# Performance work log

Measured on AMD Instinct MI355X. Metric: run time of the kernel, lower is better.

Reference implementation:

```python
import jax, jax.numpy as jnp
import numpy as np

B, E, H, L, V = 128, 1024, 1024, 2, 32001  # vocab = output_size + 1
PAD_IDX = 1000


def gru_cell(x, h, w_ih, w_hh, b_ih, b_hh):
    # PyTorch GRU cell math; gates ordered (r, z, n)
    gi = x @ w_ih.T + b_ih            # [B, 3H]
    gh = h @ w_hh.T + b_hh            # [B, 3H]
    i_r, i_z, i_n = jnp.split(gi, 3, axis=-1)
    h_r, h_z, h_n = jnp.split(gh, 3, axis=-1)
    r = jax.nn.sigmoid(i_r + h_r)
    z = jax.nn.sigmoid(i_z + h_z)
    n = jnp.tanh(i_n + r * h_n)
    return (1.0 - z) * n + z * h


def setup_inputs() -> dict:
    key = jax.random.key(0)
    ks = jax.random.split(key, 16)
    input_vector = jax.random.randint(ks[0], (B,), 0, V)
    hidden = jax.random.normal(ks[1], (L, B, H), dtype=jnp.float32)
    emb = jax.random.uniform(ks[2], (V, E), minval=-0.1, maxval=0.1, dtype=jnp.float32)
    emb = emb.at[PAD_IDX].set(0.0)  # padding_idx
    s = 1.0 / np.sqrt(H)
    def u(k, shape):
        return jax.random.uniform(k, shape, minval=-s, maxval=s, dtype=jnp.float32)
    w_ih0 = u(ks[3], (3 * H, E)); w_hh0 = u(ks[4], (3 * H, H))
    b_ih0 = u(ks[5], (3 * H,));  b_hh0 = u(ks[6], (3 * H,))
    w_ih1 = u(ks[7], (3 * H, H)); w_hh1 = u(ks[8], (3 * H, H))
    b_ih1 = u(ks[9], (3 * H,));  b_hh1 = u(ks[10], (3 * H,))
    w_out = jax.random.uniform(ks[11], (V, H), minval=-0.1, maxval=0.1, dtype=jnp.float32)
    b_out = jnp.zeros((V,), dtype=jnp.float32)
    return dict(input_vector=input_vector, hidden=hidden, emb=emb,
                w_ih0=w_ih0, w_hh0=w_hh0, b_ih0=b_ih0, b_hh0=b_hh0,
                w_ih1=w_ih1, w_hh1=w_hh1, b_ih1=b_ih1, b_hh1=b_hh1,
                w_out=w_out, b_out=b_out)


def reference(input_vector, hidden, emb, w_ih0, w_hh0, b_ih0, b_hh0,
              w_ih1, w_hh1, b_ih1, b_hh1, w_out, b_out):
    x = jax.nn.relu(emb[input_vector])          # [B, E] (seq_len=1 squeezed)
    h0 = gru_cell(x, hidden[0], w_ih0, w_hh0, b_ih0, b_hh0)   # [B, H]
    h1 = gru_cell(h0, hidden[1], w_ih1, w_hh1, b_ih1, b_hh1)  # [B, H]
    logits = h1 @ w_out.T + b_out               # [B, V]
    out = jax.nn.log_softmax(logits, axis=-1)   # [B, V]
    hidden_out = jnp.stack([h0, h1], axis=0)    # [L, B, H]
    return out, hidden_out
```

## Files before the change

### kernel.cpp

```cpp
#include <hip/hip_runtime.h>
#include <cmath>

#define BATCH 128
#define KDIM 1024
#define VOCAB 32001
#define G3 3072
#define GIP_STRIDE (BATCH * G3)

typedef __bf16 bf16_t;
typedef bf16_t bf16x8 __attribute__((ext_vector_type(8)));
typedef float f32x4 __attribute__((ext_vector_type(4)));

__device__ __forceinline__ void stage16(const float* g, void* lds_wave_base) {
    __builtin_amdgcn_global_load_lds(
        (const __attribute__((address_space(1))) void*)g,
        (__attribute__((address_space(3))) void*)lds_wave_base, 16, 0, 0);
}

template<bool RELU>
__device__ __forceinline__ bf16x8 frag_from_lds(const float* s, int row, int quad) {
    const int s7 = row & 7;
    f32x4 u = *(const f32x4*)(s + row * 32 + (((2 * quad) ^ s7) * 4));
    f32x4 v = *(const f32x4*)(s + row * 32 + (((2 * quad + 1) ^ s7) * 4));
    if (RELU) {
#pragma unroll
        for (int k = 0; k < 4; ++k) { u[k] = fmaxf(u[k], 0.f); v[k] = fmaxf(v[k], 0.f); }
    }
    bf16x8 r;
    r[0] = (bf16_t)u[0]; r[1] = (bf16_t)u[1]; r[2] = (bf16_t)u[2]; r[3] = (bf16_t)u[3];
    r[4] = (bf16_t)v[0]; r[5] = (bf16_t)v[1]; r[6] = (bf16_t)v[2]; r[7] = (bf16_t)v[3];
    return r;
}

template<bool GATHER>
__device__ __forceinline__ void gemm128_core(
    const float* __restrict__ Abase, const int* __restrict__ idx,
    const float* __restrict__ W, const float* __restrict__ bias,
    float* __restrict__ C, int ldc, int Wrows, int n0, int kbeg, int kend)
{
    __shared__ float sA[2][128 * 32];
    __shared__ float sB[2][64 * 32];
    const int t    = threadIdx.x;
    const int wave = t >> 6;
    const int lane = t & 63;
    const int l15  = lane & 15;
    const int quad = lane >> 4;
    const int wm   = wave & 1;
    const int wn   = wave >> 1;
    const int srow = t >> 3;
    const int sg   = t & 7;

    const float* aSrc[4];
#pragma unroll
    for (int r = 0; r < 4; ++r) {
        const int row = r * 32 + srow;
        const int kg  = sg ^ (row & 7);
        const float* rb = GATHER ? Abase + (size_t)idx[row] * KDIM
                                 : Abase + (size_t)row * KDIM;
        aSrc[r] = rb + kg * 4;
    }
    const float* wSrc[2];
#pragma unroll
    for (int r = 0; r < 2; ++r) {
        const int row = r * 32 + srow;
        int wr = n0 + row; if (wr > Wrows - 1) wr = Wrows - 1;
        wSrc[r] = W + (size_t)wr * KDIM + (sg ^ (row & 7)) * 4;
    }

    auto issue = [&](int k0, int buf) {
#pragma unroll
        for (int r = 0; r < 4; ++r)
            stage16(aSrc[r] + k0, (char*)&sA[buf][0] + r * 4096 + wave * 1024);
#pragma unroll
        for (int r = 0; r < 2; ++r)
            stage16(wSrc[r] + k0, (char*)&sB[buf][0] + r * 4096 + wave * 1024);
    };

    f32x4 acc[4][2];
#pragma unroll
    for (int i = 0; i < 4; ++i)
#pragma unroll
        for (int j = 0; j < 2; ++j) acc[i][j] = f32x4{0.f, 0.f, 0.f, 0.f};

    issue(kbeg, 0);
    __syncthreads();
    int buf = 0;
    for (int k0 = kbeg; k0 < kend; k0 += 32) {
        if (k0 + 32 < kend) issue(k0 + 32, buf ^ 1);
        bf16x8 bf[2];
#pragma unroll
        for (int j = 0; j < 2; ++j)
            bf[j] = frag_from_lds<false>(&sB[buf][0], wn * 32 + j * 16 + l15, quad);
#pragma unroll
        for (int i = 0; i < 4; ++i) {
            const bf16x8 af =
                frag_from_lds<GATHER>(&sA[buf][0], wm * 64 + i * 16 + l15, quad);
#pragma unroll
            for (int j = 0; j < 2; ++j)
                acc[i][j] = __builtin_amdgcn_mfma_f32_16x16x32_bf16(
                    af, bf[j], acc[i][j], 0, 0, 0);
        }
        buf ^= 1;
        __syncthreads();
    }

#pragma unroll
    for (int j = 0; j < 2; ++j) {
        const int col = n0 + wn * 32 + j * 16 + l15;
        if (col < Wrows) {
            const float bv = bias ? bias[col] : 0.f;
#pragma unroll
            for (int i = 0; i < 4; ++i)
#pragma unroll
                for (int r = 0; r < 4; ++r) {
                    const int row = wm * 64 + i * 16 + quad * 4 + r;
                    C[(size_t)row * ldc + col] = acc[i][j][r] + bv;
                }
        }
    }
}

__global__ __launch_bounds__(256) void gemm_gru0(
    const int* __restrict__ idx, const float* __restrict__ emb,
    const float* __restrict__ wih, float* __restrict__ giP,
    const float* __restrict__ hprev, const float* __restrict__ whh,
    float* __restrict__ ghP)
{
    const int split = blockIdx.x;
    const int n0    = blockIdx.y * 64;
    const int kbeg  = split * 256;
    if (blockIdx.z == 0)
        gemm128_core<true>(emb, idx, wih, nullptr, giP + (size_t)split * GIP_STRIDE,
                           G3, G3, n0, kbeg, kbeg + 256);
    else
        gemm128_core<false>(hprev, nullptr, whh, nullptr,
                            ghP + (size_t)split * GIP_STRIDE, G3, G3, n0, kbeg, kbeg + 256);
}

__global__ __launch_bounds__(256) void gemm_gru1(
    const float* __restrict__ h0, const float* __restrict__ wih,
    float* __restrict__ giP, const float* __restrict__ hprev,
    const float* __restrict__ whh, float* __restrict__ ghP)
{
    const int split = blockIdx.x;
    const int n0    = blockIdx.y * 64;
    const int kbeg  = split * 256;
    if (blockIdx.z == 0)
        gemm128_core<false>(h0, nullptr, wih, nullptr,
                            giP + (size_t)split * GIP_STRIDE, G3, G3, n0, kbeg, kbeg + 256);
    else
        gemm128_core<false>(hprev, nullptr, whh, nullptr,
                            ghP + (size_t)split * GIP_STRIDE, G3, G3, n0, kbeg, kbeg + 256);
}

__global__ __launch_bounds__(256) void gemm_vocab(
    const float* __restrict__ A, const float* __restrict__ W,
    const float* __restrict__ bias, float* __restrict__ C)
{
    gemm128_core<false>(A, nullptr, W, bias, C, VOCAB, VOCAB,
                        blockIdx.x * 64, 0, KDIM);
}

__device__ __forceinline__ f32x4 sum_splits(const float* p) {
    f32x4 s = *(const f32x4*)p;
    s += *(const f32x4*)(p + GIP_STRIDE);
    s += *(const f32x4*)(p + 2 * GIP_STRIDE);
    s += *(const f32x4*)(p + 3 * GIP_STRIDE);
    return s;
}

__global__ __launch_bounds__(256) void gru_gate(const float* __restrict__ giP,
                                                const float* __restrict__ ghP,
                                                const float* __restrict__ b_ih,
                                                const float* __restrict__ b_hh,
                                                const float* __restrict__ hprev,
                                                float* __restrict__ hout) {
    const int i  = blockIdx.x * 256 + threadIdx.x;
    const int b  = i >> 8;
    const int j  = (i & 255) * 4;
    const size_t base = (size_t)b * G3 + j;

    f32x4 ir = sum_splits(giP + base),        hr = sum_splits(ghP + base);
    f32x4 iz = sum_splits(giP + base + 1024), hz = sum_splits(ghP + base + 1024);
    f32x4 in = sum_splits(giP + base + 2048), hn = sum_splits(ghP + base + 2048);
    const f32x4 bir = *(const f32x4*)(b_ih + j);
    const f32x4 biz = *(const f32x4*)(b_ih + j + 1024);
    const f32x4 bin = *(const f32x4*)(b_ih + j + 2048);
    const f32x4 bhr = *(const f32x4*)(b_hh + j);
    const f32x4 bhz = *(const f32x4*)(b_hh + j + 1024);
    const f32x4 bhn = *(const f32x4*)(b_hh + j + 2048);
    const f32x4 hp  = *(const f32x4*)(hprev + (size_t)b * KDIM + j);

    f32x4 o;
#pragma unroll
    for (int k = 0; k < 4; ++k) {
        const float r = 1.f / (1.f + __expf(-(ir[k] + bir[k] + hr[k] + bhr[k])));
        const float z = 1.f / (1.f + __expf(-(iz[k] + biz[k] + hz[k] + bhz[k])));
        const float a = in[k] + bin[k] + r * (hn[k] + bhn[k]);
        const float n = 1.f - 2.f / (__expf(2.f * a) + 1.f);
        o[k] = (1.f - z) * n + z * hp[k];
    }
    *(f32x4*)(hout + (size_t)b * KDIM + j) = o;
}

__global__ __launch_bounds__(1024) void log_softmax_rows(float* __restrict__ out) {
    float* row = out + (size_t)blockIdx.x * VOCAB;
    const int t = threadIdx.x;
    __shared__ float sm[16], ss[16];

    float m = -3.4e38f, s = 0.f;
    for (int i = t; i < VOCAB; i += 1024) {
        const float v  = row[i];
        const float mn = fmaxf(m, v);
        s = s * __expf(m - mn) + __expf(v - mn);
        m = mn;
    }
#pragma unroll
    for (int o = 32; o; o >>= 1) {
        const float mo = __shfl_down(m, o);
        const float so = __shfl_down(s, o);
        const float mn = fmaxf(m, mo);
        s = s * __expf(m - mn) + so * __expf(mo - mn);
        m = mn;
    }
    if ((t & 63) == 0) { sm[t >> 6] = m; ss[t >> 6] = s; }
    __syncthreads();
    if (t == 0) {
        float M = sm[0], S = ss[0];
#pragma unroll
        for (int w = 1; w < 16; ++w) {
            const float mn = fmaxf(M, sm[w]);
            S = S * __expf(M - mn) + ss[w] * __expf(sm[w] - mn);
            M = mn;
        }
        sm[0] = M + __logf(S);
    }
    __syncthreads();
    const float L = sm[0];

    for (int i = t * 4; i + 3 < VOCAB; i += 4096) {
        f32x4 v = *(const f32x4*)(row + i);
        v[0] -= L; v[1] -= L; v[2] -= L; v[3] -= L;
        *(f32x4*)(row + i) = v;
    }
    if (t == 0) row[32000] -= L;
}

extern "C" void kernel_launch(void* const* d_in, const int* in_sizes, int n_in,
                              void* d_out, int out_size, void* d_ws, size_t ws_size,
                              hipStream_t stream) {
    const int*   ivec  = (const int*)  d_in[0];
    const float* hidden= (const float*)d_in[1];
    const float* emb   = (const float*)d_in[2];
    const float* w_ih0 = (const float*)d_in[3];
    const float* w_hh0 = (const float*)d_in[4];
    const float* b_ih0 = (const float*)d_in[5];
    const float* b_hh0 = (const float*)d_in[6];
    const float* w_ih1 = (const float*)d_in[7];
    const float* w_hh1 = (const float*)d_in[8];
    const float* b_ih1 = (const float*)d_in[9];
    const float* b_hh1 = (const float*)d_in[10];
    const float* w_out = (const float*)d_in[11];
    const float* b_out = (const float*)d_in[12];

    float* out = (float*)d_out;
    float* h0  = out + (size_t)BATCH * VOCAB;
    float* h1  = h0 + BATCH * KDIM;

    float* giP = out + 131072;
    float* ghP = giP + 4 * GIP_STRIDE;

    const float* hprev0 = hidden;
    const float* hprev1 = hidden + BATCH * KDIM;

    gemm_gru0<<<dim3(4, 48, 2), 256, 0, stream>>>(ivec, emb, w_ih0, giP,
                                                  hprev0, w_hh0, ghP);
    gru_gate<<<128, 256, 0, stream>>>(giP, ghP, b_ih0, b_hh0, hprev0, h0);

    gemm_gru1<<<dim3(4, 48, 2), 256, 0, stream>>>(h0, w_ih1, giP,
                                                  hprev1, w_hh1, ghP);
    gru_gate<<<128, 256, 0, stream>>>(giP, ghP, b_ih1, b_hh1, hprev1, h1);

    gemm_vocab<<<501, 256, 0, stream>>>(h1, w_out, b_out, out);

    log_softmax_rows<<<128, 1024, 0, stream>>>(out);
}
```

Measured before the change: 358.3 us.

## Pre-convert activations to bf16 and restage GEMM with 64-wide single-buffered K tiles

Adds a prep kernel that gathers the embedding rows, applies ReLU and converts them and the previous hidden states to bf16. The gate kernels now also write bf16 copies of h0/h1, so the GEMMs stage bf16 A tiles instead of converting fp32 in the inner loop. The GEMM core switches from double-buffered 32-wide K steps to single-buffered 64-wide steps with a 16-group swizzle for W and sets a launch-bounds occupancy hint. Scratch buffers move into a separate workspace. This cuts A-side bytes and per-fragment conversions, but gives up load/compute overlap inside each block and adds one extra launch.

After: 336.6 us. -6.0%, faster.

```diff
diff --git a/kernel.cpp b/kernel.cpp
--- a/kernel.cpp
+++ b/kernel.cpp
@@ -11,35 +11,20 @@
 typedef bf16_t bf16x8 __attribute__((ext_vector_type(8)));
 typedef float f32x4 __attribute__((ext_vector_type(4)));
 
-__device__ __forceinline__ void stage16(const float* g, void* lds_wave_base) {
+__device__ __forceinline__ void stage16(const void* g, void* lds) {
     __builtin_amdgcn_global_load_lds(
         (const __attribute__((address_space(1))) void*)g,
-        (__attribute__((address_space(3))) void*)lds_wave_base, 16, 0, 0);
-}
-
-template<bool RELU>
-__device__ __forceinline__ bf16x8 frag_from_lds(const float* s, int row, int quad) {
-    const int s7 = row & 7;
-    f32x4 u = *(const f32x4*)(s + row * 32 + (((2 * quad) ^ s7) * 4));
-    f32x4 v = *(const f32x4*)(s + row * 32 + (((2 * quad + 1) ^ s7) * 4));
-    if (RELU) {
-#pragma unroll
-        for (int k = 0; k < 4; ++k) { u[k] = fmaxf(u[k], 0.f); v[k] = fmaxf(v[k], 0.f); }
-    }
-    bf16x8 r;
-    r[0] = (bf16_t)u[0]; r[1] = (bf16_t)u[1]; r[2] = (bf16_t)u[2]; r[3] = (bf16_t)u[3];
-    r[4] = (bf16_t)v[0]; r[5] = (bf16_t)v[1]; r[6] = (bf16_t)v[2]; r[7] = (bf16_t)v[3];
-    return r;
-}
-
-template<bool GATHER>
-__device__ __forceinline__ void gemm128_core(
-    const float* __restrict__ Abase, const int* __restrict__ idx,
-    const float* __restrict__ W, const float* __restrict__ bias,
-    float* __restrict__ C, int ldc, int Wrows, int n0, int kbeg, int kend)
+        (__attribute__((address_space(3))) void*)lds, 16, 0, 0);
+}
+
+template<bool BIAS>
+__device__ __forceinline__ void gemm_core(
+    const bf16_t* __restrict__ A, const float* __restrict__ W,
+    const float* __restrict__ bias, float* __restrict__ C,
+    int ldc, int Wrows, int n0, int kbeg, int kend)
 {
-    __shared__ float sA[2][128 * 32];
-    __shared__ float sB[2][64 * 32];
+    __shared__ bf16_t sA[128 * 64];
+    __shared__ float  sB[64 * 64];
     const int t    = threadIdx.x;
     const int wave = t >> 6;
     const int lane = t & 63;
@@ -47,34 +32,26 @@
     const int quad = lane >> 4;
     const int wm   = wave & 1;
     const int wn   = wave >> 1;
-    const int srow = t >> 3;
-    const int sg   = t & 7;
-
-    const float* aSrc[4];
+
+    const bf16_t* aSrc[4]; int aDst[4];
 #pragma unroll
     for (int r = 0; r < 4; ++r) {
-        const int row = r * 32 + srow;
+        const int row = r * 32 + (t >> 3);
+        const int sg  = t & 7;
         const int kg  = sg ^ (row & 7);
-        const float* rb = GATHER ? Abase + (size_t)idx[row] * KDIM
-                                 : Abase + (size_t)row * KDIM;
-        aSrc[r] = rb + kg * 4;
-    }
-    const float* wSrc[2];
-#pragma unroll
-    for (int r = 0; r < 2; ++r) {
-        const int row = r * 32 + srow;
+        aSrc[r] = A + (size_t)row * KDIM + kg * 8 + kbeg;
+        aDst[r] = row * 128 + sg * 16;
+    }
+    const float* wSrc[4]; int wDst[4];
+#pragma unroll
+    for (int r = 0; r < 4; ++r) {
+        const int row = r * 16 + (t >> 4);
         int wr = n0 + row; if (wr > Wrows - 1) wr = Wrows - 1;
-        wSrc[r] = W + (size_t)wr * KDIM + (sg ^ (row & 7)) * 4;
-    }
-
-    auto issue = [&](int k0, int buf) {
-#pragma unroll
-        for (int r = 0; r < 4; ++r)
-            stage16(aSrc[r] + k0, (char*)&sA[buf][0] + r * 4096 + wave * 1024);
-#pragma unroll
-        for (int r = 0; r < 2; ++r)
-            stage16(wSrc[r] + k0, (char*)&sB[buf][0] + r * 4096 + wave * 1024);
-    };
+        const int sg = t & 15;
+        const int kg = sg ^ (row & 15);
+        wSrc[r] = W + (size_t)wr * KDIM + kg * 4 + kbeg;
+        wDst[r] = row * 256 + sg * 16;
+    }
 
     f32x4 acc[4][2];
 #pragma unroll
@@ -82,25 +59,37 @@
 #pragma unroll
         for (int j = 0; j < 2; ++j) acc[i][j] = f32x4{0.f, 0.f, 0.f, 0.f};
 
-    issue(kbeg, 0);
-    __syncthreads();
-    int buf = 0;
-    for (int k0 = kbeg; k0 < kend; k0 += 32) {
-        if (k0 + 32 < kend) issue(k0 + 32, buf ^ 1);
-        bf16x8 bf[2];
-#pragma unroll
-        for (int j = 0; j < 2; ++j)
-            bf[j] = frag_from_lds<false>(&sB[buf][0], wn * 32 + j * 16 + l15, quad);
-#pragma unroll
-        for (int i = 0; i < 4; ++i) {
-            const bf16x8 af =
-                frag_from_lds<GATHER>(&sA[buf][0], wm * 64 + i * 16 + l15, quad);
-#pragma unroll
-            for (int j = 0; j < 2; ++j)
-                acc[i][j] = __builtin_amdgcn_mfma_f32_16x16x32_bf16(
-                    af, bf[j], acc[i][j], 0, 0, 0);
+    for (int k0 = 0; k0 < kend - kbeg; k0 += 64) {
+#pragma unroll
+        for (int r = 0; r < 4; ++r) stage16(aSrc[r] + k0, (char*)sA + aDst[r]);
+#pragma unroll
+        for (int r = 0; r < 4; ++r) stage16(wSrc[r] + k0, (char*)sB + wDst[r]);
+        __syncthreads();
+#pragma unroll
+        for (int s = 0; s < 2; ++s) {
+            bf16x8 bfr[2];
+#pragma unroll
+            for (int j = 0; j < 2; ++j) {
+                const int row = wn * 32 + j * 16 + l15;
+                const int gu  = (s * 8 + 2 * quad) ^ (row & 15);
+                const f32x4 u = *(const f32x4*)((const char*)sB + row * 256 + gu * 16);
+                const f32x4 v = *(const f32x4*)((const char*)sB + row * 256 + (gu ^ 1) * 16);
+                bf16x8 b;
+                b[0] = (bf16_t)u[0]; b[1] = (bf16_t)u[1]; b[2] = (bf16_t)u[2]; b[3] = (bf16_t)u[3];
+                b[4] = (bf16_t)v[0]; b[5] = (bf16_t)v[1]; b[6] = (bf16_t)v[2]; b[7] = (bf16_t)v[3];
+                bfr[j] = b;
+            }
+#pragma unroll
+            for (int i = 0; i < 4; ++i) {
+                const int row  = wm * 64 + i * 16 + l15;
+                const int phys = (s * 4 + quad) ^ (row & 7);
+                const bf16x8 af = *(const bf16x8*)((const char*)sA + row * 128 + phys * 16);
+#pragma unroll
+                for (int j = 0; j < 2; ++j)
+                    acc[i][j] = __builtin_amdgcn_mfma_f32_16x16x32_bf16(
+                        af, bfr[j], acc[i][j], 0, 0, 0);
+            }
         }
-        buf ^= 1;
         __syncthreads();
     }
 
@@ -108,7 +97,7 @@
     for (int j = 0; j < 2; ++j) {
         const int col = n0 + wn * 32 + j * 16 + l15;
         if (col < Wrows) {
-            const float bv = bias ? bias[col] : 0.f;
+            const float bv = BIAS ? bias[col] : 0.f;
 #pragma unroll
             for (int i = 0; i < 4; ++i)
 #pragma unroll
@@ -120,45 +109,50 @@
     }
 }
 
-__global__ __launch_bounds__(256) void gemm_gru0(
-    const int* __restrict__ idx, const float* __restrict__ emb,
-    const float* __restrict__ wih, float* __restrict__ giP,
-    const float* __restrict__ hprev, const float* __restrict__ whh,
+__global__ __launch_bounds__(256, 4) void gemm_gru(
+    const bf16_t* __restrict__ Ai, const float* __restrict__ wih,
+    float* __restrict__ giP,
+    const bf16_t* __restrict__ Ah, const float* __restrict__ whh,
     float* __restrict__ ghP)
 {
     const int split = blockIdx.x;
     const int n0    = blockIdx.y * 64;
     const int kbeg  = split * 256;
     if (blockIdx.z == 0)
-        gemm128_core<true>(emb, idx, wih, nullptr, giP + (size_t)split * GIP_STRIDE,
-                           G3, G3, n0, kbeg, kbeg + 256);
+        gemm_core<false>(Ai, wih, nullptr, giP + (size_t)split * GIP_STRIDE,
+                         G3, G3, n0, kbeg, kbeg + 256);
     else
-        gemm128_core<false>(hprev, nullptr, whh, nullptr,
-                            ghP + (size_t)split * GIP_STRIDE, G3, G3, n0, kbeg, kbeg + 256);
-}
-
-__global__ __launch_bounds__(256) void gemm_gru1(
-    const float* __restrict__ h0, const float* __restrict__ wih,
-    float* __restrict__ giP, const float* __restrict__ hprev,
-    const float* __restrict__ whh, float* __restrict__ ghP)
-{
-    const int split = blockIdx.x;
-    const int n0    = blockIdx.y * 64;
-    const int kbeg  = split * 256;
-    if (blockIdx.z == 0)
-        gemm128_core<false>(h0, nullptr, wih, nullptr,
-                            giP + (size_t)split * GIP_STRIDE, G3, G3, n0, kbeg, kbeg + 256);
-    else
-        gemm128_core<false>(hprev, nullptr, whh, nullptr,
-                            ghP + (size_t)split * GIP_STRIDE, G3, G3, n0, kbeg, kbeg + 256);
-}
-
-__global__ __launch_bounds__(256) void gemm_vocab(
-    const float* __restrict__ A, const float* __restrict__ W,
+        gemm_core<false>(Ah, whh, nullptr, ghP + (size_t)split * GIP_STRIDE,
+                         G3, G3, n0, kbeg, kbeg + 256);
+}
+
+__global__ __launch_bounds__(256, 4) void gemm_vocab(
+    const bf16_t* __restrict__ A, const float* __restrict__ W,
     const float* __restrict__ bias, float* __restrict__ C)
 {
-    gemm128_core<false>(A, nullptr, W, bias, C, VOCAB, VOCAB,
-                        blockIdx.x * 64, 0, KDIM);
+    gemm_core<true>(A, W, bias, C, VOCAB, VOCAB, blockIdx.x * 64, 0, KDIM);
+}
+
+__global__ __launch_bounds__(256) void prep_bf16(const int* __restrict__ idx,
+                                                 const float* __restrict__ emb,
+                                                 const float* __restrict__ hidden,
+                                                 bf16_t* __restrict__ dst) {
+    const int i = blockIdx.x * 256 + threadIdx.x;
+    const int sec = i >> 15;
+    const int j   = i & 32767;
+    f32x4 v;
+    if (sec == 0) {
+        const int b = j >> 8, e4 = j & 255;
+        v = ((const f32x4*)(emb + (size_t)idx[b] * KDIM))[e4];
+#pragma unroll
+        for (int k = 0; k < 4; ++k) v[k] = fmaxf(v[k], 0.f);
+    } else {
+        v = ((const f32x4*)(hidden + (size_t)(sec - 1) * (BATCH * KDIM)))[j];
+    }
+    bf16_t o[4];
+#pragma unroll
+    for (int k = 0; k < 4; ++k) o[k] = (bf16_t)v[k];
+    *(uint64_t*)(dst + (size_t)i * 4) = *(const uint64_t*)o;
 }
 
 __device__ __forceinline__ f32x4 sum_splits(const float* p) {
@@ -174,7 +168,8 @@
                                                 const float* __restrict__ b_ih,
                                                 const float* __restrict__ b_hh,
                                                 const float* __restrict__ hprev,
-                                                float* __restrict__ hout) {
+                                                float* __restrict__ hout,
+                                                bf16_t* __restrict__ hout_bf16) {
     const int i  = blockIdx.x * 256 + threadIdx.x;
     const int b  = i >> 8;
     const int j  = (i & 255) * 4;
@@ -192,6 +187,7 @@
     const f32x4 hp  = *(const f32x4*)(hprev + (size_t)b * KDIM + j);
 
     f32x4 o;
+    bf16_t ob[4];
 #pragma unroll
     for (int k = 0; k < 4; ++k) {
         const float r = 1.f / (1.f + __expf(-(ir[k] + bir[k] + hr[k] + bhr[k])));
@@ -199,8 +195,10 @@
         const float a = in[k] + bin[k] + r * (hn[k] + bhn[k]);
         const float n = 1.f - 2.f / (__expf(2.f * a) + 1.f);
         o[k] = (1.f - z) * n + z * hp[k];
+        ob[k] = (bf16_t)o[k];
     }
     *(f32x4*)(hout + (size_t)b * KDIM + j) = o;
+    *(uint64_t*)(hout_bf16 + (size_t)b * KDIM + j) = *(const uint64_t*)ob;
 }
 
 __global__ __launch_bounds__(1024) void log_softmax_rows(float* __restrict__ out) {
@@ -267,21 +265,27 @@
     float* h0  = out + (size_t)BATCH * VOCAB;
     float* h1  = h0 + BATCH * KDIM;
 
-    float* giP = out + 131072;
-    float* ghP = giP + 4 * GIP_STRIDE;
+    float*  ws   = (float*)d_ws;
+    float*  giP  = ws;
+    float*  ghP  = ws + 4 * (size_t)GIP_STRIDE;
+    bf16_t* xb   = (bf16_t*)(ws + 8 * (size_t)GIP_STRIDE);
+    bf16_t* hp0b = xb   + BATCH * KDIM;
+    bf16_t* hp1b = hp0b + BATCH * KDIM;
+    bf16_t* h0b  = hp1b + BATCH * KDIM;
+    bf16_t* h1b  = h0b  + BATCH * KDIM;
 
     const float* hprev0 = hidden;
     const float* hprev1 = hidden + BATCH * KDIM;
 
-    gemm_gru0<<<dim3(4, 48, 2), 256, 0, stream>>>(ivec, emb, w_ih0, giP,
-                                                  hprev0, w_hh0, ghP);
-    gru_gate<<<128, 256, 0, stream>>>(giP, ghP, b_ih0, b_hh0, hprev0, h0);
-
-    gemm_gru1<<<dim3(4, 48, 2), 256, 0, stream>>>(h0, w_ih1, giP,
-                                                  hprev1, w_hh1, ghP);
-    gru_gate<<<128, 256, 0, stream>>>(giP, ghP, b_ih1, b_hh1, hprev1, h1);
-
-    gemm_vocab<<<501, 256, 0, stream>>>(h1, w_out, b_out, out);
+    prep_bf16<<<384, 256, 0, stream>>>(ivec, emb, hidden, xb);
+
+    gemm_gru<<<dim3(4, 48, 2), 256, 0, stream>>>(xb, w_ih0, giP, hp0b, w_hh0, ghP);
+    gru_gate<<<128, 256, 0, stream>>>(giP, ghP, b_ih0, b_hh0, hprev0, h0, h0b);
+
+    gemm_gru<<<dim3(4, 48, 2), 256, 0, stream>>>(h0b, w_ih1, giP, hp1b, w_hh1, ghP);
+    gru_gate<<<128, 256, 0, stream>>>(giP, ghP, b_ih1, b_hh1, hprev1, h1, h1b);
+
+    gemm_vocab<<<501, 256, 0, stream>>>(h1b, w_out, b_out, out);
 
     log_softmax_rows<<<128, 1024, 0, stream>>>(out);
 }
```
